# Performance work log

Measured on AMD Instinct MI355X. Metric: run time of the kernel, lower is better.

## Reference

```python
import jax, jax.numpy as jnp
import numpy as np

N = 8192
INIT_SCALE = 7.0 / 7 / 2  # mean / d / 2 from the original module


def tropical_layer(x, w):
    # x: (N, K), w: (M, K) -> (N, M) via max-plus: max_k(|x_nk| + |w_mk|)
    return jnp.max(jnp.abs(x)[:, None, :] + jnp.abs(w)[None, :, :], axis=2)


def setup_inputs() -> dict:
    key = jax.random.key(0)
    k1, k2 = jax.random.split(key)
    x = jax.random.uniform(k1, (N, 10), dtype=jnp.float32) * INIT_SCALE
    w1 = jax.random.normal(k2, (3, 10), dtype=jnp.float32) * INIT_SCALE
    return {"x": x, "w1": w1}


def reference(x, w1):
    # layer1: TAlayer(10 -> 3): (N, 3)
    out = tropical_layer(x, w1)
    # tropical self dot product: (N, N)
    dist_AB = tropical_layer(out, out)
    return dist_AB
```

## Files before the change

### kernel.cpp

```cpp
#include <hip/hip_runtime.h>


#define N_ROWS 8192
#define K_DIM 10
#define M_DIM 3

#define BJ 1024
#define BI 16

__global__ void __launch_bounds__(256) fused_dist_kernel(
        const float* __restrict__ x,
        const float* __restrict__ w,
        float4* __restrict__ dist) {
    const int tid = threadIdx.x;
    const int j4 = blockIdx.x * (BJ / 4) + tid;
    const int i0 = blockIdx.y * BI;

    float aw[M_DIM][K_DIM];
#pragma unroll
    for (int m = 0; m < M_DIM; ++m)
#pragma unroll
        for (int k = 0; k < K_DIM; ++k)
            aw[m][k] = fabsf(w[m * K_DIM + k]);

    __shared__ float so[BI][M_DIM];
    if (tid < BI) {
        const int i = i0 + tid;
        float ax[K_DIM];
#pragma unroll
        for (int k = 0; k < K_DIM; ++k) ax[k] = fabsf(x[i * K_DIM + k]);
#pragma unroll
        for (int m = 0; m < M_DIM; ++m) {
            float best = -1e30f;
#pragma unroll
            for (int k = 0; k < K_DIM; ++k) best = fmaxf(best, ax[k] + aw[m][k]);
            so[tid][m] = best;
        }
    }

    float4 xv[10];
    const float4* x4 = (const float4*)x;
#pragma unroll
    for (int q = 0; q < 10; ++q) xv[q] = x4[j4 * 10 + q];
    const float* xf = (const float*)xv;

    float ob[4][M_DIM];
#pragma unroll
    for (int t = 0; t < 4; ++t) {
#pragma unroll
        for (int m = 0; m < M_DIM; ++m) {
            float best = -1e30f;
#pragma unroll
            for (int k = 0; k < K_DIM; ++k)
                best = fmaxf(best, fabsf(xf[t * K_DIM + k]) + aw[m][k]);
            ob[t][m] = best;
        }
    }

    __syncthreads();

#pragma unroll
    for (int r = 0; r < BI; ++r) {
        const float a0 = so[r][0], a1 = so[r][1], a2 = so[r][2];
        float4 v;
        v.x = fmaxf(fmaxf(a0 + ob[0][0], a1 + ob[0][1]), a2 + ob[0][2]);
        v.y = fmaxf(fmaxf(a0 + ob[1][0], a1 + ob[1][1]), a2 + ob[1][2]);
        v.z = fmaxf(fmaxf(a0 + ob[2][0], a1 + ob[2][1]), a2 + ob[2][2]);
        v.w = fmaxf(fmaxf(a0 + ob[3][0], a1 + ob[3][1]), a2 + ob[3][2]);
        dist[(size_t)(i0 + r) * (N_ROWS / 4) + j4] = v;
    }
}

extern "C" void kernel_launch(void* const* d_in, const int* in_sizes, int n_in,
                              void* d_out, int out_size, void* d_ws, size_t ws_size,
                              hipStream_t stream) {
    const float* x = (const float*)d_in[0];
    const float* w = (const float*)d_in[1];
    (void)d_ws; (void)ws_size; (void)in_sizes; (void)n_in; (void)out_size;

    fused_dist_kernel<<<dim3(N_ROWS / BJ, N_ROWS / BI), dim3(256), 0, stream>>>(
        x, w, (float4*)d_out);
}
```

Measured before the change: 253.7 us.

## Split layer-1 into a precompute kernel and widen the distance tile per thread

```diff
diff --git a/kernel.cpp b/kernel.cpp
--- a/kernel.cpp
+++ b/kernel.cpp
@@ -5,69 +5,69 @@
 #define K_DIM 10
 #define M_DIM 3
 
-#define BJ 1024
+#define BJ 4096
 #define BI 16
 
-__global__ void __launch_bounds__(256) fused_dist_kernel(
+__global__ void __launch_bounds__(256) o_kernel(
         const float* __restrict__ x,
         const float* __restrict__ w,
+        float* __restrict__ oT) {
+    const int n = blockIdx.x * 256 + threadIdx.x;
+    if (n >= N_ROWS) return;
+
+    float ax[K_DIM];
+#pragma unroll
+    for (int k = 0; k < K_DIM; ++k) ax[k] = fabsf(x[n * K_DIM + k]);
+
+#pragma unroll
+    for (int m = 0; m < M_DIM; ++m) {
+        float best = -1e30f;
+#pragma unroll
+        for (int k = 0; k < K_DIM; ++k)
+            best = fmaxf(best, ax[k] + fabsf(w[m * K_DIM + k]));
+        oT[m * N_ROWS + n] = best;
+    }
+}
+
+__global__ void __launch_bounds__(256) dist_kernel(
+        const float* __restrict__ oT,
         float4* __restrict__ dist) {
     const int tid = threadIdx.x;
-    const int j4 = blockIdx.x * (BJ / 4) + tid;
+    const int wave = tid >> 6;
+    const int lane = tid & 63;
     const int i0 = blockIdx.y * BI;
-
-    float aw[M_DIM][K_DIM];
-#pragma unroll
-    for (int m = 0; m < M_DIM; ++m)
-#pragma unroll
-        for (int k = 0; k < K_DIM; ++k)
-            aw[m][k] = fabsf(w[m * K_DIM + k]);
+    const int j4base = blockIdx.x * (BJ / 4) + wave * 256 + lane;
 
     __shared__ float so[BI][M_DIM];
-    if (tid < BI) {
-        const int i = i0 + tid;
-        float ax[K_DIM];
-#pragma unroll
-        for (int k = 0; k < K_DIM; ++k) ax[k] = fabsf(x[i * K_DIM + k]);
-#pragma unroll
-        for (int m = 0; m < M_DIM; ++m) {
-            float best = -1e30f;
-#pragma unroll
-            for (int k = 0; k < K_DIM; ++k) best = fmaxf(best, ax[k] + aw[m][k]);
-            so[tid][m] = best;
-        }
+    if (tid < BI * M_DIM) {
+        const int r = tid & (BI - 1);
+        const int m = tid >> 4;
+        so[r][m] = oT[m * N_ROWS + i0 + r];
     }
 
-    float4 xv[10];
-    const float4* x4 = (const float4*)x;
+    const float4* oT4 = (const float4*)oT;
+    float4 om[4][M_DIM];
 #pragma unroll
-    for (int q = 0; q < 10; ++q) xv[q] = x4[j4 * 10 + q];
-    const float* xf = (const float*)xv;
-
-    float ob[4][M_DIM];
+    for (int q = 0; q < 4; ++q)
 #pragma unroll
-    for (int t = 0; t < 4; ++t) {
-#pragma unroll
-        for (int m = 0; m < M_DIM; ++m) {
-            float best = -1e30f;
-#pragma unroll
-            for (int k = 0; k < K_DIM; ++k)
-                best = fmaxf(best, fabsf(xf[t * K_DIM + k]) + aw[m][k]);
-            ob[t][m] = best;
-        }
-    }
+        for (int m = 0; m < M_DIM; ++m)
+            om[q][m] = oT4[m * (N_ROWS / 4) + j4base + q * 64];
 
     __syncthreads();
 
 #pragma unroll
     for (int r = 0; r < BI; ++r) {
         const float a0 = so[r][0], a1 = so[r][1], a2 = so[r][2];
-        float4 v;
-        v.x = fmaxf(fmaxf(a0 + ob[0][0], a1 + ob[0][1]), a2 + ob[0][2]);
-        v.y = fmaxf(fmaxf(a0 + ob[1][0], a1 + ob[1][1]), a2 + ob[1][2]);
-        v.z = fmaxf(fmaxf(a0 + ob[2][0], a1 + ob[2][1]), a2 + ob[2][2]);
-        v.w = fmaxf(fmaxf(a0 + ob[3][0], a1 + ob[3][1]), a2 + ob[3][2]);
-        dist[(size_t)(i0 + r) * (N_ROWS / 4) + j4] = v;
+        const size_t rowbase = (size_t)(i0 + r) * (N_ROWS / 4);
+#pragma unroll
+        for (int q = 0; q < 4; ++q) {
+            float4 v;
+            v.x = fmaxf(fmaxf(a0 + om[q][0].x, a1 + om[q][1].x), a2 + om[q][2].x);
+            v.y = fmaxf(fmaxf(a0 + om[q][0].y, a1 + om[q][1].y), a2 + om[q][2].y);
+            v.z = fmaxf(fmaxf(a0 + om[q][0].z, a1 + om[q][1].z), a2 + om[q][2].z);
+            v.w = fmaxf(fmaxf(a0 + om[q][0].w, a1 + om[q][1].w), a2 + om[q][2].w);
+            dist[rowbase + j4base + q * 64] = v;
+        }
     }
 }
 
@@ -76,8 +76,10 @@
                               hipStream_t stream) {
     const float* x = (const float*)d_in[0];
     const float* w = (const float*)d_in[1];
-    (void)d_ws; (void)ws_size; (void)in_sizes; (void)n_in; (void)out_size;
+    float* oT = (float*)d_ws;
+    (void)in_sizes; (void)n_in; (void)out_size; (void)ws_size;
 
-    fused_dist_kernel<<<dim3(N_ROWS / BJ, N_ROWS / BI), dim3(256), 0, stream>>>(
-        x, w, (float4*)d_out);
+    o_kernel<<<dim3(N_ROWS / 256), dim3(256), 0, stream>>>(x, w, oT);
+    dist_kernel<<<dim3(N_ROWS / BJ, N_ROWS / BI), dim3(256), 0, stream>>>(
+        oT, (float4*)d_out);
 }
```

Result: no change. 258.0 us (+1.7%).
